# Kernel tuning notes

Hardware: AMD Instinct MI355X
Metric: run time of the kernel (lower is better)

## Reference

```python
import jax, jax.numpy as jnp
import numpy as np


def setup_inputs() -> dict:
    key = jax.random.key(0)
    k1, k2, k3, k4 = jax.random.split(key, 4)
    B, N, D, d_dir = 2, 512, 512, 64
    scale_in = 1.0 / np.sqrt(D)
    scale_dir = 1.0 / np.sqrt(d_dir)
    t = jax.random.normal(k1, (B, N, D), dtype=jnp.float32)
    Wq = jax.random.normal(k2, (d_dir, D), dtype=jnp.float32) * scale_in
    Wk = jax.random.normal(k3, (d_dir, D), dtype=jnp.float32) * scale_in
    Wv = jax.random.normal(k4, (D, d_dir), dtype=jnp.float32) * scale_dir
    return {"t": t, "Wq": Wq, "Wk": Wk, "Wv": Wv}


def reference(t, Wq, Wk, Wv):
    # t: (B, N, D); Wq, Wk: (d_dir, D); Wv: (D, d_dir)
    q = jnp.einsum('bnd,ed->bne', t, Wq)  # (B, N, d_dir)
    k = jnp.einsum('bnd,ed->bne', t, Wk)  # (B, N, d_dir)
    had = q[:, :, None, :] * k[:, None, :, :]  # (B, N, N, d_dir)
    kappa = jnp.einsum('bije,de->bijd', had, Wv)  # (B, N, N, D)
    return kappa
```

## Files before the change

### kernel.cpp

```cpp
#include <hip/hip_runtime.h>
#include <hip/hip_bf16.h>

#define NB   512
#define DB   512
#define EB   64
#define JT   16
#define TPB  16
#define PR   8
#define WSTR 65

typedef __bf16 bf16x8 __attribute__((ext_vector_type(8)));
typedef float  f32x4  __attribute__((ext_vector_type(4)));

__global__ __launch_bounds__(256) void qk_proj_bf16(
    const float* __restrict__ t,
    const float* __restrict__ Wq,
    const float* __restrict__ Wk,
    const float* __restrict__ Wv,
    __bf16* __restrict__ qb,
    __bf16* __restrict__ kb,
    __bf16* __restrict__ wvb)
{
    const int blk = blockIdx.x;
    const int bn0 = blk * PR;
    const int tid = threadIdx.x;
    const int e   = tid & 63;
    const int w   = tid >> 6;

    __shared__ float wqt[64 * WSTR];
    __shared__ float wkt[64 * WSTR];

    {
        const int r = blk * 4 + w;
        wvb[r * EB + e] = (__bf16)Wv[r * EB + e];
    }

    float aq0 = 0.f, ak0 = 0.f, aq1 = 0.f, ak1 = 0.f;
    const float* __restrict__ t0 = t + (size_t)(bn0 + 2 * w) * DB;
    const float* __restrict__ t1 = t0 + DB;

    const int er = tid >> 4;
    const int dd = (tid & 15) * 4;

    for (int c = 0; c < 8; ++c) {
        const int d0 = c * 64;
        __syncthreads();

        #pragma unroll
        for (int g = 0; g < 4; ++g) {
            const int erow = er + g * 16;
            const f32x4 vq = *reinterpret_cast<const f32x4*>(Wq + (size_t)erow * DB + d0 + dd);
            const f32x4 vk = *reinterpret_cast<const f32x4*>(Wk + (size_t)erow * DB + d0 + dd);
            #pragma unroll
            for (int i = 0; i < 4; ++i) {
                wqt[(dd + i) * WSTR + erow] = vq[i];
                wkt[(dd + i) * WSTR + erow] = vk[i];
            }
        }
        __syncthreads();

        #pragma unroll 8
        for (int dp = 0; dp < 64; ++dp) {
            const float tq  = wqt[dp * WSTR + e];
            const float tk  = wkt[dp * WSTR + e];
            const float tv0 = t0[d0 + dp];
            const float tv1 = t1[d0 + dp];
            aq0 += tv0 * tq;  ak0 += tv0 * tk;
            aq1 += tv1 * tq;  ak1 += tv1 * tk;
        }
    }

    const size_t r0 = (size_t)(bn0 + 2 * w) * EB + e;
    qb[r0]      = (__bf16)aq0;
    kb[r0]      = (__bf16)ak0;
    qb[r0 + EB] = (__bf16)aq1;
    kb[r0 + EB] = (__bf16)ak1;
}

__global__ __launch_bounds__(256) void kappa_mfma(
    const __bf16* __restrict__ qb,
    const __bf16* __restrict__ kb,
    const __bf16* __restrict__ wvb,
    float* __restrict__ out)
{
    const int blk = blockIdx.x;
    const int bi  = blk >> 1;
    const int b   = bi >> 9;
    const int jt0 = (blk & 1) * TPB;
    const int w    = threadIdx.x >> 6;
    const int l    = threadIdx.x & 63;
    const int lrow = l & 15;
    const int lgrp = l >> 4;
    const int dbase = w * 128;

    __shared__ float lds[2 * 4 * JT * 128];
    float* __restrict__ wtA = lds + w * (JT * 128);
    float* __restrict__ wtB = lds + 4 * JT * 128 + w * (JT * 128);

    const bf16x8 qv0 = *reinterpret_cast<const bf16x8*>(qb + (size_t)bi * EB + lgrp * 8);
    const bf16x8 qv1 = *reinterpret_cast<const bf16x8*>(qb + (size_t)bi * EB + 32 + lgrp * 8);

    bf16x8 bfrag[8][2];
    #pragma unroll
    for (int df = 0; df < 8; ++df) {
        const int d = dbase + df * 16 + lrow;
        #pragma unroll
        for (int ks = 0; ks < 2; ++ks) {
            const bf16x8 wv = *reinterpret_cast<const bf16x8*>(
                wvb + (size_t)d * EB + ks * 32 + lgrp * 8);
            const bf16x8 qq = ks ? qv1 : qv0;
            bf16x8 f;
            #pragma unroll
            for (int x = 0; x < 8; ++x)
                f[x] = (__bf16)((float)wv[x] * (float)qq[x]);
            bfrag[df][ks] = f;
        }
    }

    const __bf16* __restrict__ kbase = kb + (size_t)b * NB * EB;

    bf16x8 kv0 = *reinterpret_cast<const bf16x8*>(kbase + (size_t)(jt0 * JT + lrow) * EB + lgrp * 8);
    bf16x8 kv1 = *reinterpret_cast<const bf16x8*>(kbase + (size_t)(jt0 * JT + lrow) * EB + 32 + lgrp * 8);

    const int r_lo = l >> 5;
    const int cc   = l & 31;

    f32x4 stage[4][8];

    #pragma unroll
    for (int t = 0; t < TPB; ++t) {
        const int slot = t & 3;

        f32x4 acc[8];
        #pragma unroll
        for (int df = 0; df < 8; ++df) {
            acc[df] = (f32x4){0.f, 0.f, 0.f, 0.f};
            acc[df] = __builtin_amdgcn_mfma_f32_16x16x32_bf16(bfrag[df][0], kv0, acc[df], 0, 0, 0);
            acc[df] = __builtin_amdgcn_mfma_f32_16x16x32_bf16(bfrag[df][1], kv1, acc[df], 0, 0, 0);
        }

        if (t + 1 < TPB) {
            const int jn = (jt0 + t + 1) * JT + lrow;
            kv0 = *reinterpret_cast<const bf16x8*>(kbase + (size_t)jn * EB + lgrp * 8);
            kv1 = *reinterpret_cast<const bf16x8*>(kbase + (size_t)jn * EB + 32 + lgrp * 8);
        }

        float* __restrict__ wtile = (t & 1) ? wtB : wtA;

        asm volatile("" ::: "memory");
        #pragma unroll
        for (int df = 0; df < 8; ++df) {
            const int sc = (df * 4 + lgrp) ^ (lrow & 7);
            *reinterpret_cast<f32x4*>(wtile + lrow * 128 + sc * 4) = acc[df];
        }
        asm volatile("" ::: "memory");

        #pragma unroll
        for (int p = 0; p < 8; ++p) {
            const int r  = 2 * p + r_lo;
            const int sc = cc ^ (r & 7);
            stage[slot][p] = *reinterpret_cast<const f32x4*>(wtile + r * 128 + sc * 4);
        }
        float* __restrict__ obase =
            out + ((size_t)bi * NB + (size_t)(jt0 + t) * JT) * DB + dbase;
        #pragma unroll
        for (int p = 0; p < 8; ++p) {
            const int r = 2 * p + r_lo;
            *reinterpret_cast<f32x4*>(obase + (size_t)r * DB + cc * 4) = stage[slot][p];
        }
    }
}

extern "C" void kernel_launch(void* const* d_in, const int* in_sizes, int n_in,
                              void* d_out, int out_size, void* d_ws, size_t ws_size,
                              hipStream_t stream) {
    const float* t  = (const float*)d_in[0];
    const float* Wq = (const float*)d_in[1];
    const float* Wk = (const float*)d_in[2];
    const float* Wv = (const float*)d_in[3];
    float* out = (float*)d_out;

    const int B = 2;

    __bf16* qb  = (__bf16*)d_ws;
    __bf16* kbf = qb + (size_t)B * NB * EB;
    __bf16* wvb = kbf + (size_t)B * NB * EB;

    qk_proj_bf16<<<dim3(128), dim3(256), 0, stream>>>(t, Wq, Wk, Wv, qb, kbf, wvb);

    kappa_mfma<<<dim3(2048), dim3(256), 0, stream>>>(qb, kbf, wvb, out);
}
```

Before: 216.5 us.

## Use 8 waves per block with block-wide LDS transpose for full-row output stores

Doubles the kappa kernel's block to 512 threads, so each wave covers 64 output columns instead of 128 and holds half the B fragments. The MFMA results go into a shared 16x512 LDS tile with a block barrier, letting each thread store complete contiguous 2KB output rows rather than per-wave 512B segments. Two LDS buffers alternate between consecutive j-tiles. The cost is a __syncthreads per tile and 64KB of LDS per block, which may limit occupancy. Write-after-read safety on each buffer relies on the barrier of the following tile.

```diff
diff --git a/kernel.cpp b/kernel.cpp
--- a/kernel.cpp
+++ b/kernel.cpp
@@ -77,7 +77,7 @@
     kb[r0 + EB] = (__bf16)ak1;
 }
 
-__global__ __launch_bounds__(256) void kappa_mfma(
+__global__ __launch_bounds__(512) void kappa_mfma(
     const __bf16* __restrict__ qb,
     const __bf16* __restrict__ kb,
     const __bf16* __restrict__ wvb,
@@ -87,22 +87,23 @@
     const int bi  = blk >> 1;
     const int b   = bi >> 9;
     const int jt0 = (blk & 1) * TPB;
-    const int w    = threadIdx.x >> 6;
-    const int l    = threadIdx.x & 63;
+    const int tid = threadIdx.x;
+    const int w    = tid >> 6;
+    const int l    = tid & 63;
     const int lrow = l & 15;
     const int lgrp = l >> 4;
-    const int dbase = w * 128;
-
-    __shared__ float lds[2 * 4 * JT * 128];
-    float* __restrict__ wtA = lds + w * (JT * 128);
-    float* __restrict__ wtB = lds + 4 * JT * 128 + w * (JT * 128);
+    const int dbase = w * 64;
+
+    __shared__ float lds[2 * JT * DB];
+    float* __restrict__ bufA = lds;
+    float* __restrict__ bufB = lds + JT * DB;
 
     const bf16x8 qv0 = *reinterpret_cast<const bf16x8*>(qb + (size_t)bi * EB + lgrp * 8);
     const bf16x8 qv1 = *reinterpret_cast<const bf16x8*>(qb + (size_t)bi * EB + 32 + lgrp * 8);
 
-    bf16x8 bfrag[8][2];
+    bf16x8 bfrag[4][2];
     #pragma unroll
-    for (int df = 0; df < 8; ++df) {
+    for (int df = 0; df < 4; ++df) {
         const int d = dbase + df * 16 + lrow;
         #pragma unroll
         for (int ks = 0; ks < 2; ++ks) {
@@ -122,51 +123,78 @@
     bf16x8 kv0 = *reinterpret_cast<const bf16x8*>(kbase + (size_t)(jt0 * JT + lrow) * EB + lgrp * 8);
     bf16x8 kv1 = *reinterpret_cast<const bf16x8*>(kbase + (size_t)(jt0 * JT + lrow) * EB + 32 + lgrp * 8);
 
-    const int r_lo = l >> 5;
-    const int cc   = l & 31;
-
-    f32x4 stage[4][8];
+    const int er = tid >> 7;
+    const int ec = tid & 127;
 
     #pragma unroll
-    for (int t = 0; t < TPB; ++t) {
-        const int slot = t & 3;
-
-        f32x4 acc[8];
-        #pragma unroll
-        for (int df = 0; df < 8; ++df) {
-            acc[df] = (f32x4){0.f, 0.f, 0.f, 0.f};
-            acc[df] = __builtin_amdgcn_mfma_f32_16x16x32_bf16(bfrag[df][0], kv0, acc[df], 0, 0, 0);
-            acc[df] = __builtin_amdgcn_mfma_f32_16x16x32_bf16(bfrag[df][1], kv1, acc[df], 0, 0, 0);
-        }
-
-        if (t + 1 < TPB) {
-            const int jn = (jt0 + t + 1) * JT + lrow;
-            kv0 = *reinterpret_cast<const bf16x8*>(kbase + (size_t)jn * EB + lgrp * 8);
-            kv1 = *reinterpret_cast<const bf16x8*>(kbase + (size_t)jn * EB + 32 + lgrp * 8);
-        }
-
-        float* __restrict__ wtile = (t & 1) ? wtB : wtA;
-
-        asm volatile("" ::: "memory");
-        #pragma unroll
-        for (int df = 0; df < 8; ++df) {
-            const int sc = (df * 4 + lgrp) ^ (lrow & 7);
-            *reinterpret_cast<f32x4*>(wtile + lrow * 128 + sc * 4) = acc[df];
-        }
-        asm volatile("" ::: "memory");
-
-        #pragma unroll
-        for (int p = 0; p < 8; ++p) {
-            const int r  = 2 * p + r_lo;
-            const int sc = cc ^ (r & 7);
-            stage[slot][p] = *reinterpret_cast<const f32x4*>(wtile + r * 128 + sc * 4);
-        }
-        float* __restrict__ obase =
-            out + ((size_t)bi * NB + (size_t)(jt0 + t) * JT) * DB + dbase;
-        #pragma unroll
-        for (int p = 0; p < 8; ++p) {
-            const int r = 2 * p + r_lo;
-            *reinterpret_cast<f32x4*>(obase + (size_t)r * DB + cc * 4) = stage[slot][p];
+    for (int t2 = 0; t2 < TPB; t2 += 2) {
+        {
+            f32x4 acc[4];
+            #pragma unroll
+            for (int df = 0; df < 4; ++df) {
+                acc[df] = (f32x4){0.f, 0.f, 0.f, 0.f};
+                acc[df] = __builtin_amdgcn_mfma_f32_16x16x32_bf16(bfrag[df][0], kv0, acc[df], 0, 0, 0);
+                acc[df] = __builtin_amdgcn_mfma_f32_16x16x32_bf16(bfrag[df][1], kv1, acc[df], 0, 0, 0);
+            }
+            {
+                const int jn = (jt0 + t2 + 1) * JT + lrow;
+                kv0 = *reinterpret_cast<const bf16x8*>(kbase + (size_t)jn * EB + lgrp * 8);
+                kv1 = *reinterpret_cast<const bf16x8*>(kbase + (size_t)jn * EB + 32 + lgrp * 8);
+            }
+            #pragma unroll
+            for (int df = 0; df < 4; ++df) {
+                const int sc = w * 16 + ((df * 4 + lgrp) ^ (lrow & 7));
+                *reinterpret_cast<f32x4*>(bufA + lrow * DB + sc * 4) = acc[df];
+            }
+            __syncthreads();
+            f32x4 ve[4];
+            #pragma unroll
+            for (int p = 0; p < 4; ++p) {
+                const int r  = p * 4 + er;
+                const int sc = (ec & ~15) | ((ec & 15) ^ (r & 7));
+                ve[p] = *reinterpret_cast<const f32x4*>(bufA + r * DB + sc * 4);
+            }
+            float* __restrict__ obase =
+                out + ((size_t)bi * NB + (size_t)(jt0 + t2) * JT) * DB;
+            #pragma unroll
+            for (int p = 0; p < 4; ++p) {
+                const int r = p * 4 + er;
+                *reinterpret_cast<f32x4*>(obase + (size_t)r * DB + ec * 4) = ve[p];
+            }
+        }
+        {
+            f32x4 acc[4];
+            #pragma unroll
+            for (int df = 0; df < 4; ++df) {
+                acc[df] = (f32x4){0.f, 0.f, 0.f, 0.f};
+                acc[df] = __builtin_amdgcn_mfma_f32_16x16x32_bf16(bfrag[df][0], kv0, acc[df], 0, 0, 0);
+                acc[df] = __builtin_amdgcn_mfma_f32_16x16x32_bf16(bfrag[df][1], kv1, acc[df], 0, 0, 0);
+            }
+            if (t2 + 2 < TPB) {
+                const int jn = (jt0 + t2 + 2) * JT + lrow;
+                kv0 = *reinterpret_cast<const bf16x8*>(kbase + (size_t)jn * EB + lgrp * 8);
+                kv1 = *reinterpret_cast<const bf16x8*>(kbase + (size_t)jn * EB + 32 + lgrp * 8);
+            }
+            #pragma unroll
+            for (int df = 0; df < 4; ++df) {
+                const int sc = w * 16 + ((df * 4 + lgrp) ^ (lrow & 7));
+                *reinterpret_cast<f32x4*>(bufB + lrow * DB + sc * 4) = acc[df];
+            }
+            __syncthreads();
+            f32x4 vo[4];
+            #pragma unroll
+            for (int p = 0; p < 4; ++p) {
+                const int r  = p * 4 + er;
+                const int sc = (ec & ~15) | ((ec & 15) ^ (r & 7));
+                vo[p] = *reinterpret_cast<const f32x4*>(bufB + r * DB + sc * 4);
+            }
+            float* __restrict__ obase =
+                out + ((size_t)bi * NB + (size_t)(jt0 + t2 + 1) * JT) * DB;
+            #pragma unroll
+            for (int p = 0; p < 4; ++p) {
+                const int r = p * 4 + er;
+                *reinterpret_cast<f32x4*>(obase + (size_t)r * DB + ec * 4) = vo[p];
+            }
         }
     }
 }
@@ -188,5 +216,5 @@
 
     qk_proj_bf16<<<dim3(128), dim3(256), 0, stream>>>(t, Wq, Wk, Wv, qb, kbf, wvb);
 
-    kappa_mfma<<<dim3(2048), dim3(256), 0, stream>>>(qb, kbf, wvb, out);
+    kappa_mfma<<<dim3(2048), dim3(512), 0, stream>>>(qb, kbf, wvb, out);
 }
```

After: 214.0 us. Within noise of the previous version (-1.1%).
